# Kernel tuning notes

Hardware: AMD Instinct MI355X
Metric: run time of the kernel (lower is better)

Reference implementation:

```python
import jax, jax.numpy as jnp
import numpy as np

D = 768
N_HEADS = 12
HEAD_DIM = 64
INNER = N_HEADS * HEAD_DIM
SCALE = HEAD_DIM ** -0.5
EPS = 1e-5


def setup_inputs() -> dict:
    key = jax.random.key(0)
    ks = jax.random.split(key, 7)
    s = 0.02
    return {
        "x": jax.random.normal(ks[0], (2, 2048, D), dtype=jnp.float32),
        "Wq": jax.random.normal(ks[1], (D, INNER), dtype=jnp.float32) * s,
        "Wk": jax.random.normal(ks[2], (D, INNER), dtype=jnp.float32) * s,
        "Wv": jax.random.normal(ks[3], (D, INNER), dtype=jnp.float32) * s,
        "Wo": jax.random.normal(ks[4], (INNER, D), dtype=jnp.float32) * s,
        "bo": jnp.zeros((D,), dtype=jnp.float32),
        "gamma": jnp.ones((D,), dtype=jnp.float32),
        "beta": jnp.zeros((D,), dtype=jnp.float32),
    }


def _layernorm(x, gamma, beta):
    mu = jnp.mean(x, axis=-1, keepdims=True)
    var = jnp.var(x, axis=-1, keepdims=True)
    return (x - mu) * jax.lax.rsqrt(var + EPS) * gamma + beta


def reference(x, Wq, Wk, Wv, Wo, bo, gamma, beta):
    b, n, _ = x.shape
    h = _layernorm(x, gamma, beta)
    # project and split heads: [b, n, inner] -> [b, h, n, d]
    def split(t):
        return t.reshape(b, n, N_HEADS, HEAD_DIM).transpose(0, 2, 1, 3)
    Q = split(h @ Wq)
    K = split(h @ Wk)
    V = split(h @ Wv)
    # NOTE: module applies softmax first, THEN multiplies probs by scale
    attn = jnp.einsum('bhid,bhjd->bhij', Q, K)
    attn = jax.nn.softmax(attn, axis=-1) * SCALE
    vals = jnp.einsum('bhij,bhjd->bhid', attn, V)
    vals = vals.transpose(0, 2, 1, 3).reshape(b, n, INNER)
    out = vals @ Wo + bo
    return x + out
```

## Files before the change

### kernel.cpp

```cpp
#include <hip/hip_runtime.h>
#include <stdint.h>

typedef __bf16 bf16;
typedef __bf16 bf16x8 __attribute__((ext_vector_type(8)));
typedef float  f32x4  __attribute__((ext_vector_type(4)));
typedef unsigned short u16x4 __attribute__((ext_vector_type(4)));
typedef unsigned int   u32x4v __attribute__((ext_vector_type(4)));

#define SEQ   2048
#define DM    768
#define NH    12
#define HD    64
#define ATT_SCALE 0.125f
#define LOG2E 1.44269504f
#define LN_EPS 1e-5f

__device__ __forceinline__ void gload16(const void* g, void* l) {
  __builtin_amdgcn_global_load_lds((const __attribute__((address_space(1))) void*)g,
                                   (__attribute__((address_space(3))) void*)l,
                                   16, 0, 0);
}

__global__ __launch_bounds__(256) void prep_kernel(
    const float* __restrict__ x, const float* __restrict__ gamma,
    const float* __restrict__ beta, bf16* __restrict__ h,
    const float* __restrict__ Wq, const float* __restrict__ Wk,
    const float* __restrict__ Wv, const float* __restrict__ Wo,
    bf16* __restrict__ Wqkvt, bf16* __restrict__ Wot)
{
  __shared__ float smem[32*33];
  int bid = blockIdx.x, t = threadIdx.x;
  if (bid < 4096) {
    const float* xr = x + (size_t)bid*DM;
    float v0 = xr[t], v1 = xr[t+256], v2 = xr[t+512];
    float s = v0+v1+v2;
    float q = v0*v0+v1*v1+v2*v2;
    #pragma unroll
    for (int m=32;m>=1;m>>=1){ s += __shfl_xor(s,m,64); q += __shfl_xor(q,m,64); }
    float* rs = smem; float* rq = smem+8;
    int w = t>>6;
    if ((t&63)==0){ rs[w]=s; rq[w]=q; }
    __syncthreads();
    float S = rs[0]+rs[1]+rs[2]+rs[3];
    float Q = rq[0]+rq[1]+rq[2]+rq[3];
    float mean = S*(1.0f/DM);
    float var  = Q*(1.0f/DM) - mean*mean;
    float rstd = rsqrtf(var + LN_EPS);
    bf16* hr = h + (size_t)bid*DM;
    hr[t]     = (bf16)((v0-mean)*rstd*gamma[t]     + beta[t]);
    hr[t+256] = (bf16)((v1-mean)*rstd*gamma[t+256] + beta[t+256]);
    hr[t+512] = (bf16)((v2-mean)*rstd*gamma[t+512] + beta[t+512]);
  } else {
    int tb = bid - 4096;
    int z = tb/576, rem = tb%576;
    int r0 = (rem/24)*32, c0 = (rem%24)*32;
    int tx = t&31, ty = t>>5;
    float (*tile)[33] = (float(*)[33])smem;
    const float* src = (z==0)?Wq:(z==1)?Wk:(z==2)?Wv:Wo;
    #pragma unroll
    for (int i=ty;i<32;i+=8) tile[i][tx] = src[(size_t)(r0+i)*DM + c0+tx];
    __syncthreads();
    bf16* dst = (z<3) ? (Wqkvt + (size_t)z*DM*DM) : Wot;
    #pragma unroll
    for (int i=ty;i<32;i+=8) dst[(size_t)(c0+i)*DM + r0+tx] = (bf16)tile[tx][i];
  }
}

template<int BM, int BN, int BK, int WM, int WN, int EPI>
__global__ __launch_bounds__(256) void gemm_bt(
    const bf16* __restrict__ A, const bf16* __restrict__ Bt, int K,
    bf16* __restrict__ qk, bf16* __restrict__ vt,
    float* __restrict__ out, const float* __restrict__ bo, const float* __restrict__ xres)
{
  constexpr int MF  = BM/(WM*16);
  constexpr int NF  = BN/(WN*16);
  constexpr int GL  = (BM+BN)*BK/2048;
  constexpr int RPI = 512/BK;
  constexpr int KKN = BK/32;
  __shared__ bf16 As[3][BM][BK];
  __shared__ bf16 Bs[3][BN][BK];
  int tid = threadIdx.x, w = tid>>6, la = tid&63;
  int bn = blockIdx.x, bm = blockIdx.y;
  int wm = w / WN, wn = w % WN;
  int g = la>>4, li = la&15;
  int sr = la / (BK/8);
  int sc = (la % (BK/8))*8;
  f32x4 acc[MF][NF] = {};
  const int KT = K/BK;

  auto stage = [&](int kt, int bb) {
    int k0 = kt*BK;
    #pragma unroll
    for (int i=0;i<BM/(RPI*4);i++){ int r0 = (i*4+w)*RPI;
      gload16(A + ((size_t)(bm*BM + r0 + sr))*K + k0 + sc, &As[bb][r0][0]); }
    #pragma unroll
    for (int i=0;i<BN/(RPI*4);i++){ int r0 = (i*4+w)*RPI;
      gload16(Bt + ((size_t)(bn*BN + r0 + sr))*K + k0 + sc, &Bs[bb][r0][0]); }
  };

  stage(0,0); stage(1,1);
  asm volatile("s_waitcnt vmcnt(%0)" :: "n"(GL) : "memory");
  __builtin_amdgcn_s_barrier();
  __builtin_amdgcn_sched_barrier(0);

  for (int kt=0; kt<KT; ++kt) {
    int bb = kt%3;
    if (kt+2 < KT) stage(kt+2, (kt+2)%3);
    #pragma unroll
    for (int kk=0;kk<KKN;kk++){
      bf16x8 af[MF], bfr[NF];
      #pragma unroll
      for (int i=0;i<MF;i++) af[i]  = *(const bf16x8*)&As[bb][wm*(BM/WM)+i*16+li][kk*32+g*8];
      #pragma unroll
      for (int j=0;j<NF;j++) bfr[j] = *(const bf16x8*)&Bs[bb][wn*(BN/WN)+j*16+li][kk*32+g*8];
      __builtin_amdgcn_s_setprio(1);
      #pragma unroll
      for (int i=0;i<MF;i++)
        #pragma unroll
        for (int j=0;j<NF;j++)
          acc[i][j] = __builtin_amdgcn_mfma_f32_16x16x32_bf16(af[i], bfr[j], acc[i][j], 0,0,0);
      __builtin_amdgcn_s_setprio(0);
    }
    if (kt+1 < KT) {
      if (kt+2 < KT) asm volatile("s_waitcnt vmcnt(%0)" :: "n"(GL) : "memory");
      else           asm volatile("s_waitcnt vmcnt(0)" ::: "memory");
      __builtin_amdgcn_s_barrier();
      __builtin_amdgcn_sched_barrier(0);
    }
  }

  #pragma unroll
  for (int i=0;i<MF;i++){
    int row0 = bm*BM + wm*(BM/WM) + i*16 + g*4;
    #pragma unroll
    for (int j=0;j<NF;j++){
      int col = bn*BN + wn*(BN/WN) + j*16 + li;
      if (EPI==0){
        if (col < 1536) {
          float qs = (col < 768) ? LOG2E : 1.0f;
          #pragma unroll
          for (int r=0;r<4;r++) qk[(size_t)(row0+r)*1536 + col] = (bf16)(acc[i][j][r]*qs);
        } else {
          int cv = col - 1536; int hh = cv>>6, dd = cv&63;
          int b_ = row0>>11,  n0 = row0&2047;
          u16x4 u;
          #pragma unroll
          for (int r=0;r<4;r++){ bf16 bv = (bf16)acc[i][j][r];
            u[r] = __builtin_bit_cast(unsigned short, bv); }
          *reinterpret_cast<u16x4*>(vt + ((size_t)((b_*NH+hh)*HD+dd))*SEQ + n0) = u;
        }
      } else {
        float bb2 = bo[col];
        #pragma unroll
        for (int r=0;r<4;r++){ size_t idx = (size_t)(row0+r)*DM + col;
          out[idx] = acc[i][j][r] + bb2 + xres[idx]; }
      }
    }
  }
}

__global__ __launch_bounds__(512) void attn_kernel(
    const bf16* __restrict__ QK, const bf16* __restrict__ Vt,
    bf16* __restrict__ vals)
{
  __shared__ bf16 Ks[2][2][64][64];
  __shared__ bf16 Vs[2][2][64][64];
  int tid=threadIdx.x, w=tid>>6, la=tid&63;
  int half = w>>2, wl = w&3;
  int id = blockIdx.x;
  int xcd = id & 7, idx = id >> 3;
  int bh  = xcd*3 + idx/16;
  int qt  = idx & 15;
  int b = bh/NH, hh = bh%NH;
  int g=la>>4, li=la&15;
  int lr=la>>3;
  int lx=li&7;
  int lcs=((la&7)^lr)*8;
  size_t qrow0=(size_t)b*SEQ + qt*128;
  int kv0 = half*1024;

  bf16x8 qf[2][2];
  #pragma unroll
  for (int qh=0;qh<2;qh++){
    const bf16* qp = QK + (qrow0 + wl*32 + qh*16 + li)*1536 + hh*64;
    qf[0][qh] = *(const bf16x8*)(qp + g*8);
    qf[1][qh] = *(const bf16x8*)(qp + 32 + g*8);
  }

  const bf16* Kbase = QK + (size_t)b*SEQ*1536 + 768 + hh*64;
  const bf16* Vbase = Vt + (size_t)(b*NH+hh)*HD*SEQ;

  auto stage = [&](int tt, int bbuf) {
    int j0 = kv0 + tt*64;
    #pragma unroll
    for (int i=0;i<2;i++){ int c=i*4+wl;
      gload16(Kbase + (size_t)(j0 + c*8 + lr)*1536 + lcs, &Ks[half][bbuf][c*8][0]);
      gload16(Vbase + (size_t)(c*8 + lr)*SEQ + j0 + lcs,  &Vs[half][bbuf][c*8][0]); }
  };

  stage(0,0);
  asm volatile("s_waitcnt vmcnt(0)" ::: "memory");
  __builtin_amdgcn_s_barrier();
  __builtin_amdgcn_sched_barrier(0);

  f32x4 o[2][4] = {};
  float lp[2][2] = {};

  for (int t=0;t<16;t++){
    int bb = t&1;
    if (t+1 < 16) stage(t+1, bb^1);
    f32x4 s[2][4] = {};
    #pragma unroll
    for (int kk=0;kk<2;kk++){
      bf16x8 kf[4];
      #pragma unroll
      for (int nf=0;nf<4;nf++){
        int row = nf*16+li;
        kf[nf] = *(const bf16x8*)((const char*)&Ks[half][bb][0][0] + row*128 + (((kk*4+g)^lx)<<4));
      }
      __builtin_amdgcn_s_setprio(1);
      #pragma unroll
      for (int nf=0;nf<4;nf++){
        s[0][nf] = __builtin_amdgcn_mfma_f32_16x16x32_bf16(kf[nf], qf[kk][0], s[0][nf], 0,0,0);
        s[1][nf] = __builtin_amdgcn_mfma_f32_16x16x32_bf16(kf[nf], qf[kk][1], s[1][nf], 0,0,0);
      }
      __builtin_amdgcn_s_setprio(0);
    }
    bf16x8 pa[2][2];
    #pragma unroll
    for (int qh=0;qh<2;qh++){
      float p[4][4];
      #pragma unroll
      for (int nf=0;nf<4;nf++)
        #pragma unroll
        for (int r=0;r<4;r++){
          p[nf][r] = __builtin_amdgcn_exp2f(s[qh][nf][r]);
          lp[qh][nf&1] += p[nf][r];
        }
      #pragma unroll
      for (int ks=0;ks<2;ks++){
        unsigned int c00,c01,c10,c11;
        asm("v_cvt_pk_bf16_f32 %0, %1, %2" : "=v"(c00) : "v"(p[2*ks  ][0]), "v"(p[2*ks  ][1]));
        asm("v_cvt_pk_bf16_f32 %0, %1, %2" : "=v"(c01) : "v"(p[2*ks  ][2]), "v"(p[2*ks  ][3]));
        asm("v_cvt_pk_bf16_f32 %0, %1, %2" : "=v"(c10) : "v"(p[2*ks+1][0]), "v"(p[2*ks+1][1]));
        asm("v_cvt_pk_bf16_f32 %0, %1, %2" : "=v"(c11) : "v"(p[2*ks+1][2]), "v"(p[2*ks+1][3]));
        asm("v_permlane32_swap_b32 %0, %1" : "+v"(c00), "+v"(c10));
        asm("v_permlane32_swap_b32 %0, %1" : "+v"(c01), "+v"(c11));
        asm("v_permlane16_swap_b32 %0, %1" : "+v"(c00), "+v"(c10));
        asm("v_permlane16_swap_b32 %0, %1" : "+v"(c01), "+v"(c11));
        u32x4v cc = {c00, c01, c10, c11};
        pa[qh][ks] = __builtin_bit_cast(bf16x8, cc);
      }
    }
    #pragma unroll
    for (int ks=0;ks<2;ks++){
      bf16x8 vb[4];
      #pragma unroll
      for (int df=0;df<4;df++){
        int row = df*16+li;
        vb[df] = *(const bf16x8*)((const char*)&Vs[half][bb][0][0] + row*128 + (((ks*4+g)^lx)<<4));
      }
      __builtin_amdgcn_s_setprio(1);
      #pragma unroll
      for (int qh=0;qh<2;qh++)
        #pragma unroll
        for (int df=0;df<4;df++)
          o[qh][df] = __builtin_amdgcn_mfma_f32_16x16x32_bf16(vb[df], pa[qh][ks], o[qh][df], 0,0,0);
      __builtin_amdgcn_s_setprio(0);
    }
    if (t+1 < 16) {
      asm volatile("s_waitcnt vmcnt(0)" ::: "memory");
      __builtin_amdgcn_s_barrier();
      __builtin_amdgcn_sched_barrier(0);
    }
  }
  float lsum[2];
  #pragma unroll
  for (int qh=0;qh<2;qh++){
    float v = lp[qh][0] + lp[qh][1];
    v += __shfl_xor(v, 16, 64);
    v += __shfl_xor(v, 32, 64);
    lsum[qh] = v;
  }
  __syncthreads();
  float* om  = (float*)&Ks[0][0][0][0];
  float* lmf = (float*)&Vs[0][0][0][0];
  if (half==1){
    #pragma unroll
    for (int qh=0;qh<2;qh++){
      int row = wl*32 + qh*16 + li;
      float* orow = om + row*64;
      #pragma unroll
      for (int df=0;df<4;df++){
        int slot = (df*4 + g) ^ (row & 15);
        *reinterpret_cast<f32x4*>(orow + slot*4) = o[qh][df];
      }
      if (g==0) lmf[row] = lsum[qh];
    }
  }
  __syncthreads();
  if (half==0){
    #pragma unroll
    for (int qh=0;qh<2;qh++){
      int row = wl*32 + qh*16 + li;
      const float* orow = om + row*64;
      float ltot = lsum[qh] + lmf[row];
      float fac = ATT_SCALE / ltot;
      bf16* vrow = vals + (qrow0 + row)*DM + hh*64;
      #pragma unroll
      for (int df=0;df<4;df++){
        int slot = (df*4 + g) ^ (row & 15);
        f32x4 pv = *reinterpret_cast<const f32x4*>(orow + slot*4);
        u16x4 u;
        #pragma unroll
        for (int r=0;r<4;r++){
          bf16 bv = (bf16)((o[qh][df][r] + pv[r]) * fac);
          u[r] = __builtin_bit_cast(unsigned short, bv);
        }
        *reinterpret_cast<u16x4*>(vrow + df*16 + g*4) = u;
      }
    }
  }
}

extern "C" void kernel_launch(void* const* d_in, const int* in_sizes, int n_in,
                              void* d_out, int out_size, void* d_ws, size_t ws_size,
                              hipStream_t stream)
{
  const float* x     = (const float*)d_in[0];
  const float* Wq    = (const float*)d_in[1];
  const float* Wk    = (const float*)d_in[2];
  const float* Wv    = (const float*)d_in[3];
  const float* Wo    = (const float*)d_in[4];
  const float* bo    = (const float*)d_in[5];
  const float* gamma = (const float*)d_in[6];
  const float* beta  = (const float*)d_in[7];
  float* out = (float*)d_out;
  char* ws = (char*)d_ws;

  bf16* h     = (bf16*)(ws + 0);
  bf16* vals  = (bf16*)(ws + 0);
  bf16* Wqkvt = (bf16*)(ws + 6291456);
  bf16* Wot   = (bf16*)(ws + 9830400);
  bf16* QKb   = (bf16*)(ws + 11010048);
  bf16* Vt    = (bf16*)(ws + 23592960);
  (void)ws_size; (void)in_sizes; (void)n_in; (void)out_size;

  prep_kernel<<<dim3(6400), dim3(256), 0, stream>>>(
      x, gamma, beta, h, Wq, Wk, Wv, Wo, Wqkvt, Wot);
  gemm_bt<128,128,32,2,2,0><<<dim3(18,32), dim3(256), 0, stream>>>(
      h, Wqkvt, DM, QKb, Vt, nullptr, nullptr, nullptr);
  attn_kernel<<<dim3(384), dim3(512), 0, stream>>>(QKb, Vt, vals);
  gemm_bt<64,64,64,2,2,1><<<dim3(12,64), dim3(256), 0, stream>>>(
      vals, Wot, DM, nullptr, nullptr, out, bo, x);
}
```

Measured before the change: 100.1 us.

## Halve attention block size and single-buffer K tiles to raise occupancy

The attention kernel now runs 256-thread blocks covering 64 query rows each instead of 512 threads covering 128, and the grid doubles to 768 blocks. This should balance work across CUs better and let more blocks sit on each CU. K tiles are now single-buffered and V tiles double-buffered inside one 48 KB shared region. The prefetch of the next K/V tile moves to after the QK^T MFMAs, behind an extra barrier. In exchange, K loads can overlap only the softmax and PV phase, and each block synchronizes one more time per tile.

```diff
diff --git a/kernel.cpp b/kernel.cpp
--- a/kernel.cpp
+++ b/kernel.cpp
@@ -159,24 +159,23 @@
   }
 }
 
-__global__ __launch_bounds__(512) void attn_kernel(
+__global__ __launch_bounds__(256) void attn_kernel(
     const bf16* __restrict__ QK, const bf16* __restrict__ Vt,
     bf16* __restrict__ vals)
 {
-  __shared__ bf16 Ks[2][2][64][64];
-  __shared__ bf16 Vs[2][2][64][64];
+  __shared__ char smem[49408];
   int tid=threadIdx.x, w=tid>>6, la=tid&63;
-  int half = w>>2, wl = w&3;
+  int half = w>>1, wl = w&1;
   int id = blockIdx.x;
   int xcd = id & 7, idx = id >> 3;
-  int bh  = xcd*3 + idx/16;
-  int qt  = idx & 15;
+  int bh  = xcd*3 + idx/32;
+  int qt  = idx & 31;
   int b = bh/NH, hh = bh%NH;
   int g=la>>4, li=la&15;
   int lr=la>>3;
   int lx=li&7;
   int lcs=((la&7)^lr)*8;
-  size_t qrow0=(size_t)b*SEQ + qt*128;
+  size_t qrow0=(size_t)b*SEQ + qt*64;
   int kv0 = half*1024;
 
   bf16x8 qf[2][2];
@@ -189,16 +188,23 @@
 
   const bf16* Kbase = QK + (size_t)b*SEQ*1536 + 768 + hh*64;
   const bf16* Vbase = Vt + (size_t)(b*NH+hh)*HD*SEQ;
-
-  auto stage = [&](int tt, int bbuf) {
+  char* kreg = smem + half*8192;
+
+  auto stageK = [&](int tt) {
     int j0 = kv0 + tt*64;
     #pragma unroll
-    for (int i=0;i<2;i++){ int c=i*4+wl;
-      gload16(Kbase + (size_t)(j0 + c*8 + lr)*1536 + lcs, &Ks[half][bbuf][c*8][0]);
-      gload16(Vbase + (size_t)(c*8 + lr)*SEQ + j0 + lcs,  &Vs[half][bbuf][c*8][0]); }
+    for (int i=0;i<4;i++){ int r0 = wl*32 + i*8;
+      gload16(Kbase + (size_t)(j0 + r0 + lr)*1536 + lcs, kreg + r0*128); }
   };
-
-  stage(0,0);
+  auto stageV = [&](int tt, int vb) {
+    int j0 = kv0 + tt*64;
+    char* vreg = smem + 16384 + (half*2+vb)*8192;
+    #pragma unroll
+    for (int i=0;i<4;i++){ int r0 = wl*32 + i*8;
+      gload16(Vbase + (size_t)(r0 + lr)*SEQ + j0 + lcs, vreg + r0*128); }
+  };
+
+  stageK(0); stageV(0,0);
   asm volatile("s_waitcnt vmcnt(0)" ::: "memory");
   __builtin_amdgcn_s_barrier();
   __builtin_amdgcn_sched_barrier(0);
@@ -207,8 +213,6 @@
   float lp[2][2] = {};
 
   for (int t=0;t<16;t++){
-    int bb = t&1;
-    if (t+1 < 16) stage(t+1, bb^1);
     f32x4 s[2][4] = {};
     #pragma unroll
     for (int kk=0;kk<2;kk++){
@@ -216,7 +220,7 @@
       #pragma unroll
       for (int nf=0;nf<4;nf++){
         int row = nf*16+li;
-        kf[nf] = *(const bf16x8*)((const char*)&Ks[half][bb][0][0] + row*128 + (((kk*4+g)^lx)<<4));
+        kf[nf] = *(const bf16x8*)(kreg + row*128 + (((kk*4+g)^lx)<<4));
       }
       __builtin_amdgcn_s_setprio(1);
       #pragma unroll
@@ -225,6 +229,11 @@
         s[1][nf] = __builtin_amdgcn_mfma_f32_16x16x32_bf16(kf[nf], qf[kk][1], s[1][nf], 0,0,0);
       }
       __builtin_amdgcn_s_setprio(0);
+    }
+    if (t+1 < 16) {
+      __builtin_amdgcn_s_barrier();
+      stageK(t+1);
+      stageV(t+1, (t+1)&1);
     }
     bf16x8 pa[2][2];
     #pragma unroll
@@ -252,13 +261,14 @@
         pa[qh][ks] = __builtin_bit_cast(bf16x8, cc);
       }
     }
+    const char* vreg = smem + 16384 + (half*2+(t&1))*8192;
     #pragma unroll
     for (int ks=0;ks<2;ks++){
       bf16x8 vb[4];
       #pragma unroll
       for (int df=0;df<4;df++){
         int row = df*16+li;
-        vb[df] = *(const bf16x8*)((const char*)&Vs[half][bb][0][0] + row*128 + (((ks*4+g)^lx)<<4));
+        vb[df] = *(const bf16x8*)(vreg + row*128 + (((ks*4+g)^lx)<<4));
       }
       __builtin_amdgcn_s_setprio(1);
       #pragma unroll
@@ -283,8 +293,8 @@
     lsum[qh] = v;
   }
   __syncthreads();
-  float* om  = (float*)&Ks[0][0][0][0];
-  float* lmf = (float*)&Vs[0][0][0][0];
+  float* om  = (float*)smem;
+  float* lmf = (float*)(smem + 49152);
   if (half==1){
     #pragma unroll
     for (int qh=0;qh<2;qh++){
@@ -350,7 +360,7 @@
       x, gamma, beta, h, Wq, Wk, Wv, Wo, Wqkvt, Wot);
   gemm_bt<128,128,32,2,2,0><<<dim3(18,32), dim3(256), 0, stream>>>(
       h, Wqkvt, DM, QKb, Vt, nullptr, nullptr, nullptr);
-  attn_kernel<<<dim3(384), dim3(512), 0, stream>>>(QKb, Vt, vals);
+  attn_kernel<<<dim3(768), dim3(256), 0, stream>>>(QKb, Vt, vals);
   gemm_bt<64,64,64,2,2,1><<<dim3(12,64), dim3(256), 0, stream>>>(
       vals, Wot, DM, nullptr, nullptr, out, bo, x);
 }
```

New measurement: 99.75 us. Within noise of the previous version (-0.3%).
